# Kernel tuning notes

Measured on AMD Instinct MI355X. Metric: run time of the kernel, lower is better.

Reference implementation:

```python
import jax, jax.numpy as jnp
import numpy as np

N, K, C, H, V = 4096, 32, 128, 128, 21   # residues, kNN, node/edge dim, hidden, vocab
NEG_SLOPE = 0.2

def gatv2(src_feat, tgt_feat, edge_feat, Wl, bl, Wr, br, We, be, att, b_out):
    # GATv2Conv (1 head, eval mode) on a regular kNN graph.
    # src_feat: [N,K,Din] gathered source-node features per edge; tgt_feat: [N,Din]
    xl = src_feat @ Wl + bl                       # [N,K,C]
    xr = tgt_feat @ Wr + br                       # [N,C]
    ee = edge_feat @ We + be                      # [N,K,C]
    m = jax.nn.leaky_relu(xl + xr[:, None, :] + ee, NEG_SLOPE)
    alpha = jax.nn.softmax(jnp.einsum('nkc,c->nk', m, att), axis=1)
    return jnp.einsum('nk,nkc->nc', alpha, xl) + b_out

def setup_inputs():
    key = jax.random.key(0)
    ks = jax.random.split(key, 32)
    w = lambda k, s: jax.random.normal(k, s, jnp.float32) * 0.05
    z0 = lambda s: jnp.zeros(s, jnp.float32)
    return dict(
        E=jax.random.normal(ks[0], (N, K, C), jnp.float32),
        E_idx=jax.random.randint(ks[1], (N, K), 0, N),
        S=jax.random.randint(ks[2], (N,), 0, V),
        mask=jnp.ones((N,), jnp.float32),
        chain_M=jnp.ones((N,), jnp.float32),
        z=jax.random.normal(ks[3], (N,), jnp.float32),
        Wl1=w(ks[4], (C, C)), bl1=z0((C,)),
        Wr1=w(ks[5], (C, C)), br1=z0((C,)),
        We1=w(ks[6], (C, C)), be1=z0((C,)),
        a1=w(ks[7], (C,)), bo1=z0((C,)),
        Wl2=w(ks[8], (C + H, C)), bl2=z0((C,)),
        Wr2=w(ks[9], (C + H, C)), br2=z0((C,)),
        We2=w(ks[10], (C, C)), be2=z0((C,)),
        a2=w(ks[11], (C,)), bo2=z0((C,)),
        W_s=w(ks[12], (V, H)),
        W_out=w(ks[13], (C, V)), b_out=z0((V,)),
    )

def reference(E, E_idx, S, mask, chain_M, z,
              Wl1, bl1, Wr1, br1, We1, be1, a1, bo1,
              Wl2, bl2, Wr2, br2, We2, be2, a2, bo2,
              W_s, W_out, b_out):
    # encoder GAT over zero-initialized node features
    x0 = jnp.zeros((N, C), E.dtype)
    node_attr = gatv2(x0[E_idx], x0, E, Wl1, bl1, Wr1, br1, We1, be1, a1, bo1)
    seq_attr = W_s[S]                                        # [N,H]
    h_full = jnp.concatenate([node_attr, seq_attr], -1)      # [N,C+H]
    h_mask = jnp.concatenate([node_attr, jnp.zeros_like(seq_attr)], -1)
    cm = chain_M * mask
    decoding_order = jnp.argsort((cm + 1e-4) * jnp.abs(z))   # [N]
    P = jax.nn.one_hot(decoding_order, N, dtype=E.dtype)     # [N,N] permutation
    L = 1.0 - jnp.triu(jnp.ones((N, N), E.dtype))            # strictly lower tri
    order_mask_backward = jnp.einsum('ij,iq,jp->qp', L, P, P)
    mask_attend = jnp.take_along_axis(order_mask_backward, E_idx, axis=1)[..., None]
    m1d = mask[:, None, None]
    mask_bw = m1d * mask_attend
    mask_fw = m1d * (1.0 - mask_attend)
    # per-edge source features: neighbor seq embedding visible only if decoded earlier
    src = h_full[E_idx] * mask_bw + h_mask[E_idx] * mask_fw  # [N,K,C+H]
    out = gatv2(src, h_mask, E, Wl2, bl2, Wr2, br2, We2, be2, a2, bo2)
    logits = out @ W_out + b_out
    return jax.nn.log_softmax(logits, axis=-1)
```

## Files before the change

### kernel.cpp

```cpp
#include <hip/hip_runtime.h>
#include <hip/hip_bf16.h>

typedef short short8 __attribute__((ext_vector_type(8)));
typedef float float4v __attribute__((ext_vector_type(4)));

#define WS_T   0
#define WS_D   2688
#define WS_C   2816
#define WS_O   2944
#define WS_A2  3072
#define WS_KEY 3200

__device__ __forceinline__ unsigned int pack2bf(float a, float b) {
  union { float f; unsigned int u; } xa, xb;
  xa.f = a; xb.f = b;
  return ((xa.u + 0x8000u) >> 16) | ((xb.u + 0x8000u) & 0xFFFF0000u);
}

__global__ __launch_bounds__(256) void pg6_pre(
    const float* __restrict__ Wl2, const float* __restrict__ Wr2,
    const float* __restrict__ We2, const float* __restrict__ bl1,
    const float* __restrict__ bl2, const float* __restrict__ br2,
    const float* __restrict__ be2, const float* __restrict__ a2,
    const float* __restrict__ bo1, const float* __restrict__ bo2,
    const float* __restrict__ W_s, const float* __restrict__ mask,
    const float* __restrict__ chain_M, const float* __restrict__ z,
    void* __restrict__ ws)
{
  short* wsW = (short*)ws;
  float* F = (float*)ws + 8192;
  const int b = blockIdx.x, tid = threadIdx.x;
  if (b == 0) {
    for (int s = tid; s < 16384; s += 256) {
      const int row = s >> 7, c = s & 127;
      const int q = row >> 5, lh = (row & 31) >> 3, j = row & 7;
      const int t = c >> 4, cl = c & 15;
      union { float f; unsigned int u; } x; x.f = We2[s];
      const unsigned int r = x.u + 0x7FFFu + ((x.u >> 16) & 1u);
      wsW[(((q * 8 + t) * 64) + lh * 16 + cl) * 8 + j] = (short)(r >> 16);
    }
    if (tid < 128) {
      const int c = tid;
      float cl0 = 0.f, cr0 = 0.f;
      for (int i = 0; i < 128; i++) {
        const float s = bl1[i] + bo1[i];
        cl0 += s * Wl2[i * 128 + c];
        cr0 += s * Wr2[i * 128 + c];
      }
      F[WS_D + c]  = be2[c] + bl2[c] + br2[c] + cr0;
      F[WS_C + c]  = cl0;
      F[WS_O + c]  = bl2[c] + bo2[c];
      F[WS_A2 + c] = a2[c];
    }
  } else if (b <= 21) {
    const int v = b - 1;
    if (tid < 128) {
      const int c = tid;
      float acc = 0.f;
      for (int h = 0; h < 128; h++)
        acc += W_s[v * 128 + h] * Wl2[(128 + h) * 128 + c];
      F[WS_T + v * 128 + c] = acc;
    }
  } else {
    const int n = (b - 22) * 256 + tid;
    F[WS_KEY + n] = (chain_M[n] * mask[n] + 1e-4f) * fabsf(z[n]);
  }
}

__global__ __launch_bounds__(256) void pg6_main(
    const float* __restrict__ E, const int* __restrict__ E_idx,
    const int* __restrict__ S, const float* __restrict__ mask,
    const float* __restrict__ W_out, const float* __restrict__ b_out,
    const void* __restrict__ ws, float* __restrict__ out)
{
  __shared__ __align__(16) short ldsW[16384];
  __shared__ float ldsTp[21 * 132];
  __shared__ float ldsD[128], ldsC[128], ldsO[128], ldsA2[128];
  __shared__ float ldswk[4][32];
  __shared__ int   ldsrv[4][32];
  __shared__ float ldsout[4][128];

  const short* wsW = (const short*)ws;
  const float* F = (const float*)ws + 8192;
  const int tid  = threadIdx.x;
  const int wave = tid >> 6;
  const int lane = tid & 63;
  const int quad = lane >> 4;
  const int lid  = lane & 15;
  const int nb   = blockIdx.x * 4;
  const int n    = nb + wave;
  const float maskn = mask[n];

  short8 afr[2][4];
#pragma unroll
  for (int g = 0; g < 2; g++) {
    const float* erow = E + (size_t)(n * 32 + g * 16 + lid) * 128 + quad * 8;
#pragma unroll
    for (int q = 0; q < 4; q++) {
      const float4 A = *(const float4*)(erow + q * 32);
      const float4 B = *(const float4*)(erow + q * 32 + 4);
      union { short8 s; unsigned int u[4]; } v;
      v.u[0] = pack2bf(A.x, A.y);
      v.u[1] = pack2bf(A.z, A.w);
      v.u[2] = pack2bf(B.x, B.y);
      v.u[3] = pack2bf(B.z, B.w);
      afr[g][q] = v.s;
    }
  }

  for (int i = tid * 8; i < 16384; i += 2048)
    *(uint4*)&ldsW[i] = *(const uint4*)&wsW[i];
  for (int idx = tid; idx < 2688; idx += 256) {
    const int v = idx >> 7, c = idx & 127;
    ldsTp[v * 132 + c] = F[WS_T + idx];
  }
  if (tid < 128) {
    ldsD[tid]  = F[WS_D + tid];
    ldsC[tid]  = F[WS_C + tid];
    ldsO[tid]  = F[WS_O + tid];
    ldsA2[tid] = F[WS_A2 + tid];
  }
  if (tid < 128) {
    const int w = tid >> 5, k = tid & 31, nn = nb + w;
    const int j = E_idx[nn * 32 + k];
    const float keyn = F[WS_KEY + nn], kj = F[WS_KEY + j];
    const int before = (kj < keyn) || (kj == keyn && j < nn);
    ldswk[w][k] = before ? mask[nn] : 0.f;
    ldsrv[w][k] = S[j];
  }
  __syncthreads();

  float dv[8], a2v[8];
#pragma unroll
  for (int t = 0; t < 8; t++) {
    const int c = t * 16 + lid;
    dv[t]  = ldsD[c] + maskn * ldsC[c];
    a2v[t] = ldsA2[c];
  }
  int rows[2][4]; float wks[2][4];
#pragma unroll
  for (int g = 0; g < 2; g++)
#pragma unroll
    for (int r = 0; r < 4; r++) {
      const int kk = g * 16 + quad * 4 + r;
      rows[g][r] = ldsrv[wave][kk] * 132;
      wks[g][r]  = ldswk[wave][kk];
    }

  float sreg[2][4];
#pragma unroll
  for (int g = 0; g < 2; g++) {
    float part[4] = {0.f, 0.f, 0.f, 0.f};
#pragma unroll
    for (int t = 0; t < 8; t++) {
      float4v acc = {0.f, 0.f, 0.f, 0.f};
#pragma unroll
      for (int q = 0; q < 4; q++) {
        const short8 bfr = *(const short8*)&ldsW[(((q * 8 + t) * 64) + lane) * 8];
        acc = __builtin_amdgcn_mfma_f32_16x16x32_bf16(afr[g][q], bfr, acc, 0, 0, 0);
      }
      const int c = t * 16 + lid;
#pragma unroll
      for (int r = 0; r < 4; r++) {
        float val = acc[r] + dv[t] + wks[g][r] * ldsTp[rows[g][r] + c];
        val = fmaxf(val, 0.f) + 0.2f * fminf(val, 0.f);
        part[r] = fmaf(val, a2v[t], part[r]);
      }
    }
#pragma unroll
    for (int r = 0; r < 4; r++) {
      float v = part[r];
      v += __shfl_xor(v, 1);
      v += __shfl_xor(v, 2);
      v += __shfl_xor(v, 4);
      v += __shfl_xor(v, 8);
      sreg[g][r] = v;
    }
  }

  float mx = -1e30f;
#pragma unroll
  for (int g = 0; g < 2; g++)
#pragma unroll
    for (int r = 0; r < 4; r++) mx = fmaxf(mx, sreg[g][r]);
  mx = fmaxf(mx, __shfl_xor(mx, 16));
  mx = fmaxf(mx, __shfl_xor(mx, 32));
  float eg[2][4], esum = 0.f;
#pragma unroll
  for (int g = 0; g < 2; g++)
#pragma unroll
    for (int r = 0; r < 4; r++) {
      eg[g][r] = expf(sreg[g][r] - mx);
      esum += eg[g][r];
    }
  esum += __shfl_xor(esum, 16);
  esum += __shfl_xor(esum, 32);
  const float inv = 1.f / esum;
  float cg[2][4];
#pragma unroll
  for (int g = 0; g < 2; g++)
#pragma unroll
    for (int r = 0; r < 4; r++) cg[g][r] = eg[g][r] * inv * wks[g][r];

  float o0 = ldsO[lane]      + maskn * ldsC[lane];
  float o1 = ldsO[lane + 64] + maskn * ldsC[lane + 64];
#pragma unroll
  for (int kk = 0; kk < 32; kk++) {
    const int g = kk >> 4, sq = (kk >> 2) & 3, r = kk & 3;
    const float cf = __shfl(cg[g][r], sq * 16);
    const int row = ldsrv[wave][kk] * 132;
    o0 = fmaf(cf, ldsTp[row + lane], o0);
    o1 = fmaf(cf, ldsTp[row + lane + 64], o1);
  }
  ldsout[wave][lane]      = o0;
  ldsout[wave][lane + 64] = o1;
  __syncthreads();

  float l0 = 0.f, l1 = 0.f, l2 = 0.f, l3 = 0.f;
  if (lane < 21) {
    const float* wo = W_out + lane;
#pragma unroll 8
    for (int c = 0; c < 128; c += 4) {
      l0 = fmaf(ldsout[wave][c],     wo[c * 21],       l0);
      l1 = fmaf(ldsout[wave][c + 1], wo[(c + 1) * 21], l1);
      l2 = fmaf(ldsout[wave][c + 2], wo[(c + 2) * 21], l2);
      l3 = fmaf(ldsout[wave][c + 3], wo[(c + 3) * 21], l3);
    }
  }
  float lg = (lane < 21) ? (b_out[lane] + ((l0 + l1) + (l2 + l3))) : -1e30f;
  float lmx = lg;
  lmx = fmaxf(lmx, __shfl_xor(lmx, 1));
  lmx = fmaxf(lmx, __shfl_xor(lmx, 2));
  lmx = fmaxf(lmx, __shfl_xor(lmx, 4));
  lmx = fmaxf(lmx, __shfl_xor(lmx, 8));
  lmx = fmaxf(lmx, __shfl_xor(lmx, 16));
  float ex = (lane < 21) ? expf(lg - lmx) : 0.f;
  float es = ex;
  es += __shfl_xor(es, 1);
  es += __shfl_xor(es, 2);
  es += __shfl_xor(es, 4);
  es += __shfl_xor(es, 8);
  es += __shfl_xor(es, 16);
  if (lane < 21)
    out[n * 21 + lane] = lg - lmx - logf(es);
}

extern "C" void kernel_launch(void* const* d_in, const int* in_sizes, int n_in,
                              void* d_out, int out_size, void* d_ws, size_t ws_size,
                              hipStream_t stream)
{
  const float* E       = (const float*)d_in[0];
  const int*   E_idx   = (const int*)d_in[1];
  const int*   S       = (const int*)d_in[2];
  const float* mask    = (const float*)d_in[3];
  const float* chain_M = (const float*)d_in[4];
  const float* z       = (const float*)d_in[5];
  const float* bl1     = (const float*)d_in[7];
  const float* bo1     = (const float*)d_in[13];
  const float* Wl2     = (const float*)d_in[14];
  const float* bl2     = (const float*)d_in[15];
  const float* Wr2     = (const float*)d_in[16];
  const float* br2     = (const float*)d_in[17];
  const float* We2     = (const float*)d_in[18];
  const float* be2     = (const float*)d_in[19];
  const float* a2      = (const float*)d_in[20];
  const float* bo2     = (const float*)d_in[21];
  const float* W_s     = (const float*)d_in[22];
  const float* W_out   = (const float*)d_in[23];
  const float* b_out   = (const float*)d_in[24];

  pg6_pre<<<38, 256, 0, stream>>>(Wl2, Wr2, We2, bl1, bl2, br2, be2, a2,
                                  bo1, bo2, W_s, mask, chain_M, z, d_ws);
  pg6_main<<<1024, 256, 0, stream>>>(E, E_idx, S, mask, W_out, b_out, d_ws,
                                     (float*)d_out);
}
```

Measured before the change: 171.9 us.

## Read weights and tables directly from global memory instead of staging in LDS

Removes the per-block staging of the packed bf16 weight matrix, the T table and the bias vectors into shared memory. Each wave now reads the MFMA B fragments and the table values straight from global memory, relying on L1/L2 caching. Block-wide syncthreads become wave barriers, and both 16-row groups share one set of B fragment loads per column tile. This shrinks LDS use (raising occupancy) and removes the block-level sync, but adds latency and traffic on the global/cache path.

```diff
diff --git a/kernel.cpp b/kernel.cpp
--- a/kernel.cpp
+++ b/kernel.cpp
@@ -17,7 +17,7 @@
   return ((xa.u + 0x8000u) >> 16) | ((xb.u + 0x8000u) & 0xFFFF0000u);
 }
 
-__global__ __launch_bounds__(256) void pg6_pre(
+__global__ __launch_bounds__(256) void pg7_pre(
     const float* __restrict__ Wl2, const float* __restrict__ Wr2,
     const float* __restrict__ We2, const float* __restrict__ bl1,
     const float* __restrict__ bl2, const float* __restrict__ br2,
@@ -67,18 +67,15 @@
   }
 }
 
-__global__ __launch_bounds__(256) void pg6_main(
+__global__ __launch_bounds__(256) void pg7_main(
     const float* __restrict__ E, const int* __restrict__ E_idx,
     const int* __restrict__ S, const float* __restrict__ mask,
     const float* __restrict__ W_out, const float* __restrict__ b_out,
     const void* __restrict__ ws, float* __restrict__ out)
 {
-  __shared__ __align__(16) short ldsW[16384];
-  __shared__ float ldsTp[21 * 132];
-  __shared__ float ldsD[128], ldsC[128], ldsO[128], ldsA2[128];
+  __shared__ float ldsout[4][128];
   __shared__ float ldswk[4][32];
   __shared__ int   ldsrv[4][32];
-  __shared__ float ldsout[4][128];
 
   const short* wsW = (const short*)ws;
   const float* F = (const float*)ws + 8192;
@@ -87,9 +84,17 @@
   const int lane = tid & 63;
   const int quad = lane >> 4;
   const int lid  = lane & 15;
-  const int nb   = blockIdx.x * 4;
-  const int n    = nb + wave;
+  const int n    = blockIdx.x * 4 + wave;
   const float maskn = mask[n];
+
+  if (lane < 32) {
+    const int j = E_idx[n * 32 + lane];
+    const float keyn = F[WS_KEY + n], kj = F[WS_KEY + j];
+    const int before = (kj < keyn) || (kj == keyn && j < n);
+    ldswk[wave][lane] = before ? maskn : 0.f;
+    ldsrv[wave][lane] = S[j] * 128;
+  }
+  __builtin_amdgcn_wave_barrier();
 
   short8 afr[2][4];
 #pragma unroll
@@ -108,75 +113,54 @@
     }
   }
 
-  for (int i = tid * 8; i < 16384; i += 2048)
-    *(uint4*)&ldsW[i] = *(const uint4*)&wsW[i];
-  for (int idx = tid; idx < 2688; idx += 256) {
-    const int v = idx >> 7, c = idx & 127;
-    ldsTp[v * 132 + c] = F[WS_T + idx];
-  }
-  if (tid < 128) {
-    ldsD[tid]  = F[WS_D + tid];
-    ldsC[tid]  = F[WS_C + tid];
-    ldsO[tid]  = F[WS_O + tid];
-    ldsA2[tid] = F[WS_A2 + tid];
-  }
-  if (tid < 128) {
-    const int w = tid >> 5, k = tid & 31, nn = nb + w;
-    const int j = E_idx[nn * 32 + k];
-    const float keyn = F[WS_KEY + nn], kj = F[WS_KEY + j];
-    const int before = (kj < keyn) || (kj == keyn && j < nn);
-    ldswk[w][k] = before ? mask[nn] : 0.f;
-    ldsrv[w][k] = S[j];
-  }
-  __syncthreads();
-
-  float dv[8], a2v[8];
+  int rows[2][4]; float wks[2][4];
+#pragma unroll
+  for (int g = 0; g < 2; g++)
+#pragma unroll
+    for (int r = 0; r < 4; r++) {
+      const int kk = g * 16 + quad * 4 + r;
+      rows[g][r] = ldsrv[wave][kk];
+      wks[g][r]  = ldswk[wave][kk];
+    }
+
+  float part[2][4] = {{0.f, 0.f, 0.f, 0.f}, {0.f, 0.f, 0.f, 0.f}};
 #pragma unroll
   for (int t = 0; t < 8; t++) {
+    short8 bfr[4];
+#pragma unroll
+    for (int q = 0; q < 4; q++)
+      bfr[q] = *(const short8*)(wsW + (((q * 8 + t) * 64) + lane) * 8);
+    float4v ac0 = {0.f, 0.f, 0.f, 0.f}, ac1 = {0.f, 0.f, 0.f, 0.f};
+#pragma unroll
+    for (int q = 0; q < 4; q++) {
+      ac0 = __builtin_amdgcn_mfma_f32_16x16x32_bf16(afr[0][q], bfr[q], ac0, 0, 0, 0);
+      ac1 = __builtin_amdgcn_mfma_f32_16x16x32_bf16(afr[1][q], bfr[q], ac1, 0, 0, 0);
+    }
     const int c = t * 16 + lid;
-    dv[t]  = ldsD[c] + maskn * ldsC[c];
-    a2v[t] = ldsA2[c];
-  }
-  int rows[2][4]; float wks[2][4];
-#pragma unroll
-  for (int g = 0; g < 2; g++)
-#pragma unroll
-    for (int r = 0; r < 4; r++) {
-      const int kk = g * 16 + quad * 4 + r;
-      rows[g][r] = ldsrv[wave][kk] * 132;
-      wks[g][r]  = ldswk[wave][kk];
-    }
-
+    const float dvt  = F[WS_D + c] + maskn * F[WS_C + c];
+    const float a2vt = F[WS_A2 + c];
+#pragma unroll
+    for (int r = 0; r < 4; r++) {
+      float v0 = ac0[r] + dvt + wks[0][r] * F[WS_T + rows[0][r] + c];
+      float v1 = ac1[r] + dvt + wks[1][r] * F[WS_T + rows[1][r] + c];
+      v0 = fmaxf(v0, 0.f) + 0.2f * fminf(v0, 0.f);
+      v1 = fmaxf(v1, 0.f) + 0.2f * fminf(v1, 0.f);
+      part[0][r] = fmaf(v0, a2vt, part[0][r]);
+      part[1][r] = fmaf(v1, a2vt, part[1][r]);
+    }
+  }
   float sreg[2][4];
 #pragma unroll
-  for (int g = 0; g < 2; g++) {
-    float part[4] = {0.f, 0.f, 0.f, 0.f};
-#pragma unroll
-    for (int t = 0; t < 8; t++) {
-      float4v acc = {0.f, 0.f, 0.f, 0.f};
-#pragma unroll
-      for (int q = 0; q < 4; q++) {
-        const short8 bfr = *(const short8*)&ldsW[(((q * 8 + t) * 64) + lane) * 8];
-        acc = __builtin_amdgcn_mfma_f32_16x16x32_bf16(afr[g][q], bfr, acc, 0, 0, 0);
-      }
-      const int c = t * 16 + lid;
-#pragma unroll
-      for (int r = 0; r < 4; r++) {
-        float val = acc[r] + dv[t] + wks[g][r] * ldsTp[rows[g][r] + c];
-        val = fmaxf(val, 0.f) + 0.2f * fminf(val, 0.f);
-        part[r] = fmaf(val, a2v[t], part[r]);
-      }
-    }
-#pragma unroll
-    for (int r = 0; r < 4; r++) {
-      float v = part[r];
+  for (int g = 0; g < 2; g++)
+#pragma unroll
+    for (int r = 0; r < 4; r++) {
+      float v = part[g][r];
       v += __shfl_xor(v, 1);
       v += __shfl_xor(v, 2);
       v += __shfl_xor(v, 4);
       v += __shfl_xor(v, 8);
       sreg[g][r] = v;
     }
-  }
 
   float mx = -1e30f;
 #pragma unroll
@@ -202,19 +186,19 @@
 #pragma unroll
     for (int r = 0; r < 4; r++) cg[g][r] = eg[g][r] * inv * wks[g][r];
 
-  float o0 = ldsO[lane]      + maskn * ldsC[lane];
-  float o1 = ldsO[lane + 64] + maskn * ldsC[lane + 64];
+  float o0 = F[WS_O + lane]      + maskn * F[WS_C + lane];
+  float o1 = F[WS_O + lane + 64] + maskn * F[WS_C + lane + 64];
 #pragma unroll
   for (int kk = 0; kk < 32; kk++) {
     const int g = kk >> 4, sq = (kk >> 2) & 3, r = kk & 3;
     const float cf = __shfl(cg[g][r], sq * 16);
-    const int row = ldsrv[wave][kk] * 132;
-    o0 = fmaf(cf, ldsTp[row + lane], o0);
-    o1 = fmaf(cf, ldsTp[row + lane + 64], o1);
+    const int row = ldsrv[wave][kk];
+    o0 = fmaf(cf, F[WS_T + row + lane], o0);
+    o1 = fmaf(cf, F[WS_T + row + lane + 64], o1);
   }
   ldsout[wave][lane]      = o0;
   ldsout[wave][lane + 64] = o1;
-  __syncthreads();
+  __builtin_amdgcn_wave_barrier();
 
   float l0 = 0.f, l1 = 0.f, l2 = 0.f, l3 = 0.f;
   if (lane < 21) {
@@ -269,8 +253,8 @@
   const float* W_out   = (const float*)d_in[23];
   const float* b_out   = (const float*)d_in[24];
 
-  pg6_pre<<<38, 256, 0, stream>>>(Wl2, Wr2, We2, bl1, bl2, br2, be2, a2,
+  pg7_pre<<<38, 256, 0, stream>>>(Wl2, Wr2, We2, bl1, bl2, br2, be2, a2,
                                   bo1, bo2, W_s, mask, chain_M, z, d_ws);
-  pg6_main<<<1024, 256, 0, stream>>>(E, E_idx, S, mask, W_out, b_out, d_ws,
+  pg7_main<<<1024, 256, 0, stream>>>(E, E_idx, S, mask, W_out, b_out, d_ws,
                                      (float*)d_out);
 }
```

Result: no change. 173.0 us (+0.6%).
